# Kernel optimization log

Measured on AMD Instinct MI355X. Metric: run time of the kernel, lower is better.

The kernel has to match this reference:

```python
import jax, jax.numpy as jnp
import numpy as np

ALPHA = 0.2
NEG_INF = -9e15


def setup_inputs() -> dict:
    key = jax.random.key(0)
    k1, k2, k3, k4 = jax.random.split(key, 4)
    N, F_IN, F_OUT, H = 4096, 1, 64, 12
    x = jax.random.normal(k1, (N, F_IN), dtype=jnp.float32)
    adj = jax.random.randint(k2, (N, N), 0, 2).astype(jnp.int32)
    # per-head params stacked: W [H, F_IN, F_OUT], a [H, 2*F_OUT, 1]
    W = jax.random.normal(k3, (H, F_IN, F_OUT), dtype=jnp.float32) * 0.1
    a = jax.random.normal(k4, (H, 2 * F_OUT, 1), dtype=jnp.float32) * 0.1
    return {"x": x, "adj": adj, "W": W, "a": a}


def reference(x, adj, W, a):
    # h per head: [H, N, F_OUT]
    h = jnp.einsum('nf,hfo->hno', x, W)
    F_out = h.shape[-1]
    # a_input[i,j] = concat(h_i, h_j), so a_input @ a = h_i.a_src + h_j.a_dst
    a_src = a[:, :F_out, 0]   # [H, F_OUT]
    a_dst = a[:, F_out:, 0]   # [H, F_OUT]
    e_src = jnp.einsum('hnf,hf->hn', h, a_src)  # [H, N]
    e_dst = jnp.einsum('hnf,hf->hn', h, a_dst)  # [H, N]
    e = jax.nn.leaky_relu(e_src[:, :, None] + e_dst[:, None, :], ALPHA)  # [H,N,N]
    e = jnp.where(adj[None] > 0, e, NEG_INF)
    attn = jax.nn.softmax(e, axis=-1)           # softmax over neighbors j
    h_prime = jnp.einsum('hij,hjf->hif', attn, h)  # [H, N, F_OUT]
    # concat heads along feature dim -> [N, H*F_OUT]
    N = h_prime.shape[1]
    return jnp.transpose(h_prime, (1, 0, 2)).reshape(N, -1)
```

## Files before the change

kernel.cpp:

```cpp
#include <hip/hip_runtime.h>

#define GAT_H 12
#define GAT_N 4096
#define GAT_F 64
#define LOG2E 1.4426950408889634f

__global__ __launch_bounds__(64) void gat_prep(const float* __restrict__ W,
                                               const float* __restrict__ a,
                                               const float* __restrict__ x,
                                               float* __restrict__ sd) {
    const int b = blockIdx.x;
    const int f = threadIdx.x;
    if (b < GAT_H) {
        const float wf = W[b * GAT_F + f];
        float ps = wf * a[b * 2 * GAT_F + f];
        float pd = wf * a[b * 2 * GAT_F + GAT_F + f];
        #pragma unroll
        for (int off = 32; off > 0; off >>= 1) {
            ps += __shfl_xor(ps, off, 64);
            pd += __shfl_xor(pd, off, 64);
        }
        if (f == 0) { sd[b] = ps; sd[GAT_H + b] = pd; }
    } else {
        float s = 0.0f;
        #pragma unroll
        for (int j = 0; j < GAT_N / 64; ++j) s += x[j * 64 + f];
        #pragma unroll
        for (int off = 32; off > 0; off >>= 1) s += __shfl_xor(s, off, 64);
        if (f == 0) sd[2 * GAT_H] = s * (1.0f / GAT_N);
    }
}

__global__ __launch_bounds__(256) void gat_main(const float* __restrict__ x,
                                                const int* __restrict__ adj,
                                                const float* __restrict__ W,
                                                const float* __restrict__ sd,
                                                float* __restrict__ out) {
    __shared__ float xs[GAT_N];
    const int tid = threadIdx.x;
    #pragma unroll
    for (int it = 0; it < GAT_N / (256 * 4); ++it) {
        ((float4*)xs)[it * 256 + tid] = ((const float4*)x)[it * 256 + tid];
    }
    __syncthreads();

    const int lane = tid & 63;
    const int wave = tid >> 6;
    const int row  = blockIdx.x * 4 + wave;
    const float xi = xs[row];

    float b1[GAT_H], d1[GAT_H];
    #pragma unroll
    for (int h = 0; h < GAT_H; ++h) {
        b1[h] = xi * sd[h] * LOG2E;
        d1[h] = sd[GAT_H + h] * LOG2E;
    }
    float den[GAT_H], num[GAT_H];
    #pragma unroll
    for (int h = 0; h < GAT_H; ++h) { den[h] = 0.0f; num[h] = 0.0f; }

    const int4*   __restrict__ adjrow = (const int4*)(adj + (size_t)row * GAT_N);
    const float4* __restrict__ xs4    = (const float4*)xs;

    int4   a4 = adjrow[lane];
    float4 x4 = xs4[lane];
    #pragma unroll 1
    for (int it = 0; it < 16; ++it) {
        const int nxt = (it < 15 ? it + 1 : 15) * 64 + lane;
        int4   a4n = adjrow[nxt];
        float4 x4n = xs4[nxt];
        #pragma unroll
        for (int e = 0; e < 4; ++e) {
            const int   ai = (e == 0) ? a4.x : (e == 1) ? a4.y : (e == 2) ? a4.z : a4.w;
            const float xj = (e == 0) ? x4.x : (e == 1) ? x4.y : (e == 2) ? x4.z : x4.w;
            const bool msk = ai > 0;
            #pragma unroll
            for (int h = 0; h < GAT_H; ++h) {
                float q   = fmaf(xj, d1[h], b1[h]);
                float arg = fmaxf(q, 0.2f * q);
                arg = msk ? arg : -12800.0f;
                float p = __builtin_amdgcn_exp2f(arg);
                den[h] += p;
                num[h] = fmaf(p, xj, num[h]);
            }
        }
        a4 = a4n; x4 = x4n;
    }

    #pragma unroll
    for (int h = 0; h < GAT_H; ++h) {
        #pragma unroll
        for (int off = 32; off > 0; off >>= 1) {
            den[h] += __shfl_xor(den[h], off, 64);
            num[h] += __shfl_xor(num[h], off, 64);
        }
    }

    const float xmean = sd[2 * GAT_H];
    const size_t base = (size_t)row * (GAT_H * GAT_F);
    #pragma unroll
    for (int h = 0; h < GAT_H; ++h) {
        const float c = den[h] > 0.0f ? num[h] / den[h] : xmean;
        out[base + h * GAT_F + lane] = c * W[h * GAT_F + lane];
    }
}

extern "C" void kernel_launch(void* const* d_in, const int* in_sizes, int n_in,
                              void* d_out, int out_size, void* d_ws, size_t ws_size,
                              hipStream_t stream) {
    const float* x   = (const float*)d_in[0];
    const int*   adj = (const int*)d_in[1];
    const float* W   = (const float*)d_in[2];
    const float* a   = (const float*)d_in[3];
    float* out = (float*)d_out;
    float* sd  = (float*)d_ws;

    gat_prep<<<13, 64, 0, stream>>>(W, a, x, sd);
    gat_main<<<GAT_N / 4, 256, 0, stream>>>(x, adj, W, sd, out);
}
```

Measured before the change: 133.3 us.

## Split each row across two waves and rewrite leaky-relu mask as FMAs

Each attention row is now handled by two waves, each covering half of the neighbor columns. Their partial softmax sums are combined through shared memory, and the grid doubles to N/2 blocks. The leaky-relu and mask are rewritten as 0.6*q + 0.4*|q| + mask bias, which removes the select and max from the inner loop. This adds more waves for latency hiding but costs two block barriers and restages the xs load per block twice as often.

```diff
diff --git a/kernel.cpp b/kernel.cpp
--- a/kernel.cpp
+++ b/kernel.cpp
@@ -3,6 +3,7 @@
 #define GAT_H 12
 #define GAT_N 4096
 #define GAT_F 64
+#define GAT_HALF 2048
 #define LOG2E 1.4426950408889634f
 
 __global__ __launch_bounds__(64) void gat_prep(const float* __restrict__ W,
@@ -37,6 +38,9 @@
                                                 const float* __restrict__ sd,
                                                 float* __restrict__ out) {
     __shared__ float xs[GAT_N];
+    __shared__ float part[2][2][GAT_H][2];
+    __shared__ float cbuf[2][GAT_H];
+
     const int tid = threadIdx.x;
     #pragma unroll
     for (int it = 0; it < GAT_N / (256 * 4); ++it) {
@@ -46,7 +50,9 @@
 
     const int lane = tid & 63;
     const int wave = tid >> 6;
-    const int row  = blockIdx.x * 4 + wave;
+    const int rloc = wave >> 1;
+    const int half = wave & 1;
+    const int row  = blockIdx.x * 2 + rloc;
     const float xi = xs[row];
 
     float b1[GAT_H], d1[GAT_H];
@@ -59,27 +65,28 @@
     #pragma unroll
     for (int h = 0; h < GAT_H; ++h) { den[h] = 0.0f; num[h] = 0.0f; }
 
-    const int4*   __restrict__ adjrow = (const int4*)(adj + (size_t)row * GAT_N);
-    const float4* __restrict__ xs4    = (const float4*)xs;
+    const int4*   __restrict__ adjrow =
+        (const int4*)(adj + (size_t)row * GAT_N + half * GAT_HALF);
+    const float4* __restrict__ xs4 = (const float4*)(xs + half * GAT_HALF);
 
     int4   a4 = adjrow[lane];
     float4 x4 = xs4[lane];
     #pragma unroll 1
-    for (int it = 0; it < 16; ++it) {
-        const int nxt = (it < 15 ? it + 1 : 15) * 64 + lane;
+    for (int it = 0; it < 8; ++it) {
+        const int nxt = (it < 7 ? it + 1 : 7) * 64 + lane;
         int4   a4n = adjrow[nxt];
         float4 x4n = xs4[nxt];
         #pragma unroll
         for (int e = 0; e < 4; ++e) {
             const int   ai = (e == 0) ? a4.x : (e == 1) ? a4.y : (e == 2) ? a4.z : a4.w;
             const float xj = (e == 0) ? x4.x : (e == 1) ? x4.y : (e == 2) ? x4.z : x4.w;
-            const bool msk = ai > 0;
+            const float mb = (ai > 0) ? 0.0f : -12800.0f;
             #pragma unroll
             for (int h = 0; h < GAT_H; ++h) {
-                float q   = fmaf(xj, d1[h], b1[h]);
-                float arg = fmaxf(q, 0.2f * q);
-                arg = msk ? arg : -12800.0f;
-                float p = __builtin_amdgcn_exp2f(arg);
+                const float q   = fmaf(xj, d1[h], b1[h]);
+                const float t   = fmaf(0.6f, q, mb);
+                const float arg = fmaf(0.4f, fabsf(q), t);
+                const float p   = __builtin_amdgcn_exp2f(arg);
                 den[h] += p;
                 num[h] = fmaf(p, xj, num[h]);
             }
@@ -95,13 +102,32 @@
             num[h] += __shfl_xor(num[h], off, 64);
         }
     }
+    if (lane == 0) {
+        #pragma unroll
+        for (int h = 0; h < GAT_H; ++h) {
+            part[rloc][half][h][0] = den[h];
+            part[rloc][half][h][1] = num[h];
+        }
+    }
+    __syncthreads();
 
-    const float xmean = sd[2 * GAT_H];
-    const size_t base = (size_t)row * (GAT_H * GAT_F);
+    if (tid < 2 * GAT_H) {
+        const int r = (tid >= GAT_H) ? 1 : 0;
+        const int h = tid - r * GAT_H;
+        const float dsum = part[r][0][h][0] + part[r][1][h][0];
+        const float nsum = part[r][0][h][1] + part[r][1][h][1];
+        cbuf[r][h] = dsum > 0.0f ? nsum / dsum : sd[2 * GAT_H];
+    }
+    __syncthreads();
+
     #pragma unroll
-    for (int h = 0; h < GAT_H; ++h) {
-        const float c = den[h] > 0.0f ? num[h] / den[h] : xmean;
-        out[base + h * GAT_F + lane] = c * W[h * GAT_F + lane];
+    for (int r = 0; r < 2; ++r) {
+        const size_t base = (size_t)(blockIdx.x * 2 + r) * (GAT_H * GAT_F);
+        #pragma unroll
+        for (int k = 0; k < 3; ++k) {
+            const int pos = k * 256 + tid;
+            out[base + pos] = cbuf[r][pos >> 6] * W[pos];
+        }
     }
 }
 
@@ -116,5 +142,5 @@
     float* sd  = (float*)d_ws;
 
     gat_prep<<<13, 64, 0, stream>>>(W, a, x, sd);
-    gat_main<<<GAT_N / 4, 256, 0, stream>>>(x, adj, W, sd, out);
+    gat_main<<<GAT_N / 2, 256, 0, stream>>>(x, adj, W, sd, out);
 }
```

Result: faster. 127.7 us (-4.2%).

## Factor exp of leaky-relu into precomputed per-node exponential tables

Applied to the files above, without the earlier changes.

Splits exp2(leaky(zi+zj)) into a product of per-row and per-column exponentials, picking the branch by comparing xj against a per-row threshold. A new kernel precomputes per-column exp pairs for each head, which are staged through padded LDS tiles. Each wave now handles two rows, so the inner loop replaces a transcendental with a select and a multiply. It also software-prefetches the adjacency and table tiles. The trade-offs are no max-subtraction (overflow risk for large values), an extra launch, LDS traffic and more registers.

```diff
diff --git a/kernel.cpp b/kernel.cpp
--- a/kernel.cpp
+++ b/kernel.cpp
@@ -3,7 +3,10 @@
 #define GAT_H 12
 #define GAT_N 4096
 #define GAT_F 64
+#define TJ    256
+#define NTILE (GAT_N / TJ)
 #define LOG2E 1.4426950408889634f
+#define TAB_OFF 1024
 
 __global__ __launch_bounds__(64) void gat_prep(const float* __restrict__ W,
                                                const float* __restrict__ a,
@@ -31,77 +34,150 @@
     }
 }
 
+__global__ __launch_bounds__(256) void gat_tab(const float* __restrict__ x,
+                                               const float* __restrict__ sd,
+                                               float2* __restrict__ tab) {
+    const int t  = blockIdx.x * 256 + threadIdx.x;
+    const int h  = t % GAT_H;
+    const int jg = t / GAT_H;
+    const float d = sd[GAT_H + h];
+    const float q = LOG2E * d * x[jg];
+    const float B = __builtin_amdgcn_exp2f(q);
+    const float D = __builtin_amdgcn_exp2f(0.2f * q);
+    tab[t] = (d > 0.0f) ? make_float2(B, D) : make_float2(D, B);
+}
+
 __global__ __launch_bounds__(256) void gat_main(const float* __restrict__ x,
                                                 const int* __restrict__ adj,
                                                 const float* __restrict__ W,
                                                 const float* __restrict__ sd,
+                                                const float2* __restrict__ tab,
                                                 float* __restrict__ out) {
-    __shared__ float xs[GAT_N];
-    const int tid = threadIdx.x;
-    #pragma unroll
-    for (int it = 0; it < GAT_N / (256 * 4); ++it) {
-        ((float4*)xs)[it * 256 + tid] = ((const float4*)x)[it * 256 + tid];
-    }
-    __syncthreads();
+    __shared__ float  xs[GAT_N];
+    __shared__ float2 tileb[TJ * 13];
 
+    const int tid  = threadIdx.x;
     const int lane = tid & 63;
     const int wave = tid >> 6;
-    const int row  = blockIdx.x * 4 + wave;
-    const float xi = xs[row];
 
-    float b1[GAT_H], d1[GAT_H];
     #pragma unroll
-    for (int h = 0; h < GAT_H; ++h) {
-        b1[h] = xi * sd[h] * LOG2E;
-        d1[h] = sd[GAT_H + h] * LOG2E;
-    }
-    float den[GAT_H], num[GAT_H];
-    #pragma unroll
-    for (int h = 0; h < GAT_H; ++h) { den[h] = 0.0f; num[h] = 0.0f; }
+    for (int it = 0; it < GAT_N / (256 * 4); ++it)
+        ((float4*)xs)[it * 256 + tid] = ((const float4*)x)[it * 256 + tid];
 
-    const int4*   __restrict__ adjrow = (const int4*)(adj + (size_t)row * GAT_N);
-    const float4* __restrict__ xs4    = (const float4*)xs;
+    const int row0 = blockIdx.x * 8 + wave * 2;
 
-    int4   a4 = adjrow[lane];
-    float4 x4 = xs4[lane];
-    #pragma unroll 1
-    for (int it = 0; it < 16; ++it) {
-        const int nxt = (it < 15 ? it + 1 : 15) * 64 + lane;
-        int4   a4n = adjrow[nxt];
-        float4 x4n = xs4[nxt];
+    float Av[2][GAT_H], Cv[2][GAT_H], Uv[2][GAT_H];
+    {
         #pragma unroll
-        for (int e = 0; e < 4; ++e) {
-            const int   ai = (e == 0) ? a4.x : (e == 1) ? a4.y : (e == 2) ? a4.z : a4.w;
-            const float xj = (e == 0) ? x4.x : (e == 1) ? x4.y : (e == 2) ? x4.z : x4.w;
-            const bool msk = ai > 0;
+        for (int r = 0; r < 2; ++r) {
+            const float xi = x[row0 + r];
             #pragma unroll
             for (int h = 0; h < GAT_H; ++h) {
-                float q   = fmaf(xj, d1[h], b1[h]);
-                float arg = fmaxf(q, 0.2f * q);
-                arg = msk ? arg : -12800.0f;
-                float p = __builtin_amdgcn_exp2f(arg);
-                den[h] += p;
-                num[h] = fmaf(p, xj, num[h]);
+                const float dh = sd[GAT_H + h];
+                const float zi = xi * sd[h];
+                const float A  = __builtin_amdgcn_exp2f(LOG2E * zi);
+                const float C  = __builtin_amdgcn_exp2f(0.2f * LOG2E * zi);
+                Uv[r][h] = -zi * __builtin_amdgcn_rcpf(dh);
+                const bool dp = dh > 0.0f;
+                Av[r][h] = dp ? A : C;
+                Cv[r][h] = dp ? C : A;
             }
-        }
-        a4 = a4n; x4 = x4n;
-    }
-
-    #pragma unroll
-    for (int h = 0; h < GAT_H; ++h) {
-        #pragma unroll
-        for (int off = 32; off > 0; off >>= 1) {
-            den[h] += __shfl_xor(den[h], off, 64);
-            num[h] += __shfl_xor(num[h], off, 64);
         }
     }
 
+    float den[2][GAT_H], num[2][GAT_H];
+    #pragma unroll
+    for (int r = 0; r < 2; ++r)
+        #pragma unroll
+        for (int h = 0; h < GAT_H; ++h) { den[r][h] = 0.0f; num[r][h] = 0.0f; }
+
+    int lidx[12];
+    #pragma unroll
+    for (int k = 0; k < 12; ++k) {
+        const int p = k * 256 + tid;
+        lidx[k] = (p / GAT_H) * 13 + (p % GAT_H);
+    }
+
+    float2 st[12];
+    #pragma unroll
+    for (int k = 0; k < 12; ++k) st[k] = tab[k * 256 + tid];
+
+    int acur[2][4], anxt[2][4] = {{0,0,0,0},{0,0,0,0}};
+    #pragma unroll
+    for (int r = 0; r < 2; ++r)
+        #pragma unroll
+        for (int e = 0; e < 4; ++e)
+            acur[r][e] = adj[(size_t)(row0 + r) * GAT_N + e * 64 + lane];
+
+    __syncthreads();
+
+    for (int T = 0; T < NTILE; ++T) {
+        #pragma unroll
+        for (int k = 0; k < 12; ++k) tileb[lidx[k]] = st[k];
+        __syncthreads();
+
+        if (T < NTILE - 1) {
+            const float2* g = tab + (T + 1) * (TJ * GAT_H);
+            #pragma unroll
+            for (int k = 0; k < 12; ++k) st[k] = g[k * 256 + tid];
+            const int jb = (T + 1) * TJ;
+            #pragma unroll
+            for (int r = 0; r < 2; ++r)
+                #pragma unroll
+                for (int e = 0; e < 4; ++e)
+                    anxt[r][e] = adj[(size_t)(row0 + r) * GAT_N + jb + e * 64 + lane];
+        }
+
+        #pragma unroll
+        for (int e = 0; e < 4; ++e) {
+            const int   jl = e * 64 + lane;
+            const float xj = xs[T * TJ + jl];
+            float m01[2], xm[2];
+            #pragma unroll
+            for (int r = 0; r < 2; ++r) {
+                const bool mk = acur[r][e] > 0;
+                m01[r] = mk ? 1.0f : 0.0f;
+                xm[r]  = mk ? xj   : 0.0f;
+            }
+            const float2* rowp = tileb + jl * 13;
+            #pragma unroll
+            for (int h = 0; h < GAT_H; ++h) {
+                const float2 P = rowp[h];
+                #pragma unroll
+                for (int r = 0; r < 2; ++r) {
+                    const bool  sl = xj > Uv[r][h];
+                    const float E  = sl ? P.x : P.y;
+                    const float G  = sl ? Av[r][h] : Cv[r][h];
+                    const float p  = E * G;
+                    den[r][h] = fmaf(p, m01[r], den[r][h]);
+                    num[r][h] = fmaf(p, xm[r],  num[r][h]);
+                }
+            }
+        }
+        __syncthreads();
+
+        #pragma unroll
+        for (int r = 0; r < 2; ++r)
+            #pragma unroll
+            for (int e = 0; e < 4; ++e)
+                acur[r][e] = anxt[r][e];
+    }
+
     const float xmean = sd[2 * GAT_H];
-    const size_t base = (size_t)row * (GAT_H * GAT_F);
     #pragma unroll
-    for (int h = 0; h < GAT_H; ++h) {
-        const float c = den[h] > 0.0f ? num[h] / den[h] : xmean;
-        out[base + h * GAT_F + lane] = c * W[h * GAT_F + lane];
+    for (int r = 0; r < 2; ++r) {
+        const size_t base = (size_t)(row0 + r) * (GAT_H * GAT_F);
+        #pragma unroll
+        for (int h = 0; h < GAT_H; ++h) {
+            float dn = den[r][h], nm = num[r][h];
+            #pragma unroll
+            for (int off = 32; off > 0; off >>= 1) {
+                dn += __shfl_xor(dn, off, 64);
+                nm += __shfl_xor(nm, off, 64);
+            }
+            const float c = dn > 0.0f ? nm * __builtin_amdgcn_rcpf(dn) : xmean;
+            out[base + h * GAT_F + lane] = c * W[h * GAT_F + lane];
+        }
     }
 }
 
@@ -114,7 +190,9 @@
     const float* a   = (const float*)d_in[3];
     float* out = (float*)d_out;
     float* sd  = (float*)d_ws;
+    float2* tab = (float2*)((float*)d_ws + TAB_OFF);
 
     gat_prep<<<13, 64, 0, stream>>>(W, a, x, sd);
-    gat_main<<<GAT_N / 4, 256, 0, stream>>>(x, adj, W, sd, out);
+    gat_tab<<<(GAT_N * GAT_H) / 256, 256, 0, stream>>>(x, sd, tab);
+    gat_main<<<GAT_N / 8, 256, 0, stream>>>(x, adj, W, sd, tab, out);
 }
```

Result: slower. 165.2 us (+23.9%).
